# Performance work log

Hardware: AMD Instinct MI355X
Metric: run time of the kernel (lower is better)

Reference implementation:

```python
import jax, jax.numpy as jnp
import numpy as np

N_NODES = 50000
N_EDGES = 800000
N_GRAPHS = 2500
IN_DIM = 128
HID = 64
HEADS = 2
NEG_SLOPE = 0.2


def _gat_layer(x, W, att_src, att_dst, bias, src, dst, n):
    # W: [F_in, H*C], att_*: [H, C], bias: [C]
    h = (x @ W).reshape(n, HEADS, HID)            # [N,H,C]
    a_src = jnp.sum(h * att_src[None], axis=-1)   # [N,H]
    a_dst = jnp.sum(h * att_dst[None], axis=-1)   # [N,H]
    e = jax.nn.leaky_relu(a_src[src] + a_dst[dst], NEG_SLOPE)  # [E,H]
    # segment softmax over destination neighborhoods
    m = jax.ops.segment_max(e, dst, num_segments=n)            # [N,H]
    m = jnp.where(jnp.isfinite(m), m, 0.0)
    ex = jnp.exp(e - m[dst])
    s = jax.ops.segment_sum(ex, dst, num_segments=n)           # [N,H]
    alpha = ex / jnp.maximum(s[dst], 1e-16)                    # [E,H]
    msg = h[src] * alpha[:, :, None]                           # [E,H,C]
    out = jax.ops.segment_sum(msg, dst, num_segments=n)        # [N,H,C]
    return out.mean(axis=1) + bias                             # concat=False -> head mean


def _with_self_loops(edge_index, n):
    loop = jnp.arange(n, dtype=edge_index.dtype)
    src = jnp.concatenate([edge_index[0], loop])
    dst = jnp.concatenate([edge_index[1], loop])
    return src, dst


def setup_inputs() -> dict:
    key = jax.random.key(0)
    ks = jax.random.split(key, 16)
    x = jax.random.normal(ks[0], (N_NODES, IN_DIM), dtype=jnp.float32)
    edge_index = jax.random.randint(ks[1], (2, N_EDGES), 0, N_NODES, dtype=jnp.int32)
    batch = jnp.sort(jax.random.randint(ks[2], (N_NODES,), 0, N_GRAPHS, dtype=jnp.int32))

    def glorot(k, shape):
        fan = shape[0] + shape[-1]
        return jax.random.normal(k, shape, dtype=jnp.float32) * np.sqrt(2.0 / fan)

    inp = {"x": x, "edge_index": edge_index, "batch": batch}
    dims = [IN_DIM, HID, HID]
    for i in range(3):
        inp[f"W{i+1}"] = glorot(ks[3 + 4 * i], (dims[i], HEADS * HID))
        inp[f"att_src{i+1}"] = glorot(ks[4 + 4 * i], (HEADS, HID))
        inp[f"att_dst{i+1}"] = glorot(ks[5 + 4 * i], (HEADS, HID))
        inp[f"b{i+1}"] = jnp.zeros((HID,), dtype=jnp.float32)
    inp["lin_w"] = glorot(ks[15], (HID, 1))
    inp["lin_b"] = jnp.zeros((1,), dtype=jnp.float32)
    return inp


def reference(x, W1, att_src1, att_dst1, b1, W2, att_src2, att_dst2, b2,
              W3, att_src3, att_dst3, b3, lin_w, lin_b, edge_index, batch):
    n = x.shape[0]
    src, dst = _with_self_loops(edge_index, n)
    h = jax.nn.relu(_gat_layer(x, W1, att_src1, att_dst1, b1, src, dst, n))
    h = jax.nn.relu(_gat_layer(h, W2, att_src2, att_dst2, b2, src, dst, n))
    h = jax.nn.relu(_gat_layer(h, W3, att_src3, att_dst3, b3, src, dst, n))
    # global mean pool over graphs
    sums = jax.ops.segment_sum(h, batch, num_segments=N_GRAPHS)          # [G,C]
    cnt = jax.ops.segment_sum(jnp.ones((n,), h.dtype), batch, num_segments=N_GRAPHS)
    pooled = sums / jnp.maximum(cnt, 1.0)[:, None]
    return pooled @ lin_w + lin_b                                        # [G,1]
```

## Files before the change

kernel.cpp:

```cpp
#include <hip/hip_runtime.h>
#include <hip/hip_fp16.h>
#include <math.h>


__device__ __forceinline__ float lrelu(float v) { return v > 0.f ? v : 0.2f * v; }

__device__ __forceinline__ float wave_max(float v) {
  for (int off = 32; off; off >>= 1) v = fmaxf(v, __shfl_xor(v, off, 64));
  return v;
}
__device__ __forceinline__ float half_sum(float v) {
  for (int off = 16; off; off >>= 1) v += __shfl_xor(v, off, 64);
  return v;
}
__device__ __forceinline__ float half_max(float v) {
  for (int off = 16; off; off >>= 1) v = fmaxf(v, __shfl_xor(v, off, 64));
  return v;
}

__global__ void count_rank(const int* __restrict__ ei, int* __restrict__ deg,
                           int* __restrict__ rank, int e) {
  int j0 = blockIdx.x * 1024 + threadIdx.x;
#pragma unroll
  for (int k = 0; k < 4; ++k) {
    int j = j0 + k * 256;
    if (j < e) rank[j] = atomicAdd(&deg[ei[e + j]], 1);
  }
}

__global__ void scan_blocks(const int* __restrict__ deg, int* __restrict__ row_ptr,
                            int* __restrict__ btot, int n) {
  __shared__ int sm[256];
  int i = blockIdx.x * 256 + threadIdx.x;
  int v = (i < n) ? deg[i] : 0;
  sm[threadIdx.x] = v;
  __syncthreads();
  for (int off = 1; off < 256; off <<= 1) {
    int t = (threadIdx.x >= off) ? sm[threadIdx.x - off] : 0;
    __syncthreads();
    sm[threadIdx.x] += t;
    __syncthreads();
  }
  if (i < n) row_ptr[i] = sm[threadIdx.x] - v;
  if (threadIdx.x == 255) btot[blockIdx.x] = sm[255];
}

__global__ void scan_totals(int* __restrict__ btot, int nb) {
  __shared__ int sm[256];
  int v = (threadIdx.x < nb) ? btot[threadIdx.x] : 0;
  sm[threadIdx.x] = v;
  __syncthreads();
  for (int off = 1; off < 256; off <<= 1) {
    int t = (threadIdx.x >= off) ? sm[threadIdx.x - off] : 0;
    __syncthreads();
    sm[threadIdx.x] += t;
    __syncthreads();
  }
  if (threadIdx.x < nb) btot[threadIdx.x] = sm[threadIdx.x] - v;
}

__global__ void scan_add(int* __restrict__ row_ptr, int* __restrict__ csr,
                         const int* __restrict__ btot, int n, int total) {
  int i = blockIdx.x * 256 + threadIdx.x;
  if (i < n) {
    int v = row_ptr[i] + btot[blockIdx.x] + i;
    row_ptr[i] = v;
    csr[v] = i;
  }
  if (i == 0) row_ptr[n] = total;
}

__global__ void place_kernel(const int* __restrict__ ei, const int* __restrict__ rank,
                             const int* __restrict__ row_ptr, int* __restrict__ csr,
                             int e) {
  int j0 = blockIdx.x * 1024 + threadIdx.x;
#pragma unroll
  for (int k = 0; k < 4; ++k) {
    int j = j0 + k * 256;
    if (j < e) {
      int d = ei[e + j];
      csr[row_ptr[d] + 1 + rank[j]] = ei[j];
    }
  }
}

template <int K>
__global__ __launch_bounds__(256) void gemm_att(const float* __restrict__ X,
                                                const float* __restrict__ W,
                                                const float* __restrict__ asw,
                                                const float* __restrict__ adw,
                                                __half* __restrict__ H16,
                                                float* __restrict__ a_src,
                                                float* __restrict__ a_dst, int N) {
  __shared__ float Xs[64 * 68];
  int tid = threadIdx.x;
  int row0 = blockIdx.x * 64;
  int head = blockIdx.y;
  int cgrp = tid & 15;
  int rg = tid >> 4;
  int c0 = head * 64 + cgrp * 4;
  float acc[4][4] = {};

  for (int kc = 0; kc < K; kc += 64) {
    for (int idx = tid; idx < 64 * 64; idx += 256) {
      int r = idx >> 6;
      int k = idx & 63;
      int gr = row0 + r;
      if (gr >= N) gr = N - 1;
      Xs[r * 68 + k] = X[(size_t)gr * K + kc + k];
    }
    __syncthreads();

    const float* wp = W + (size_t)kc * 128 + c0;
#pragma unroll 2
    for (int k = 0; k < 64; k += 4) {
      float4 xr[4];
#pragma unroll
      for (int j = 0; j < 4; ++j)
        xr[j] = *(const float4*)(&Xs[(rg * 4 + j) * 68 + k]);
#pragma unroll
      for (int kk = 0; kk < 4; ++kk) {
        float4 w4 = *(const float4*)(wp + (k + kk) * 128);
#pragma unroll
        for (int j = 0; j < 4; ++j) {
          float xv = ((const float*)&xr[j])[kk];
          acc[j][0] = fmaf(xv, w4.x, acc[j][0]);
          acc[j][1] = fmaf(xv, w4.y, acc[j][1]);
          acc[j][2] = fmaf(xv, w4.z, acc[j][2]);
          acc[j][3] = fmaf(xv, w4.w, acc[j][3]);
        }
      }
    }
    __syncthreads();
  }

  float4 aw = *(const float4*)(asw + c0);
  float4 dw = *(const float4*)(adw + c0);
#pragma unroll
  for (int j = 0; j < 4; ++j) {
    int r = row0 + rg * 4 + j;
    float sp = acc[j][0] * aw.x + acc[j][1] * aw.y + acc[j][2] * aw.z + acc[j][3] * aw.w;
    float dp = acc[j][0] * dw.x + acc[j][1] * dw.y + acc[j][2] * dw.z + acc[j][3] * dw.w;
#pragma unroll
    for (int off = 1; off < 16; off <<= 1) {
      sp += __shfl_xor(sp, off, 64);
      dp += __shfl_xor(dp, off, 64);
    }
    if (r < N) {
      union { __half2 h2[2]; uint2 u; } pk;
      pk.h2[0] = __floats2half2_rn(acc[j][0], acc[j][1]);
      pk.h2[1] = __floats2half2_rn(acc[j][2], acc[j][3]);
      *(uint2*)(H16 + (size_t)r * 128 + c0) = pk.u;
      if (cgrp == 0) {
        a_src[r * 2 + head] = sp;
        a_dst[r * 2 + head] = dp;
      }
    }
  }
}

__device__ __forceinline__ void ld_grp8(const __half* __restrict__ H16, int half_,
                                        int c8, int headsel, int sub, int s,
                                        float p0, float p1, int g,
                                        uint4* h, float* q) {
#pragma unroll
  for (int k = 0; k < 4; ++k) {
    int idx = half_ + g * 8 + k * 2 + sub;
    int st = __shfl(s, idx, 64);
    float q0 = __shfl(p0, idx, 64);
    float q1 = __shfl(p1, idx, 64);
    q[k] = headsel ? q1 : q0;
    h[k] = *(const uint4*)(H16 + (size_t)st * 128 + c8);
  }
}
__device__ __forceinline__ void fma_grp8(const uint4* h, const float* q,
                                         float* acc) {
#pragma unroll
  for (int k = 0; k < 4; ++k) {
    union { uint u; __half2 h2; } a, b, c, d;
    a.u = h[k].x; b.u = h[k].y; c.u = h[k].z; d.u = h[k].w;
    float2 f0 = __half22float2(a.h2);
    float2 f1 = __half22float2(b.h2);
    float2 f2 = __half22float2(c.h2);
    float2 f3 = __half22float2(d.h2);
    acc[0] = fmaf(f0.x, q[k], acc[0]);
    acc[1] = fmaf(f0.y, q[k], acc[1]);
    acc[2] = fmaf(f1.x, q[k], acc[2]);
    acc[3] = fmaf(f1.y, q[k], acc[3]);
    acc[4] = fmaf(f2.x, q[k], acc[4]);
    acc[5] = fmaf(f2.y, q[k], acc[5]);
    acc[6] = fmaf(f3.x, q[k], acc[6]);
    acc[7] = fmaf(f3.y, q[k], acc[7]);
  }
}
__device__ __forceinline__ void gather_pipe8(const __half* __restrict__ H16, int half_,
                                             int c8, int headsel, int sub, int s,
                                             float p0, float p1, int maxcnt,
                                             float* acc) {
  int groups = (maxcnt + 7) >> 3;
  uint4 ha[4], hb[4];
  float qa[4], qb[4];
  ld_grp8(H16, half_, c8, headsel, sub, s, p0, p1, 0, ha, qa);
  int g = 1;
  for (; g + 1 < groups; g += 2) {
    ld_grp8(H16, half_, c8, headsel, sub, s, p0, p1, g, hb, qb);
    fma_grp8(ha, qa, acc);
    ld_grp8(H16, half_, c8, headsel, sub, s, p0, p1, g + 1, ha, qa);
    fma_grp8(hb, qb, acc);
  }
  if (g < groups) {
    ld_grp8(H16, half_, c8, headsel, sub, s, p0, p1, g, hb, qb);
    fma_grp8(ha, qa, acc);
    fma_grp8(hb, qb, acc);
  } else {
    fma_grp8(ha, qa, acc);
  }
}

template <int POOL>
__global__ __launch_bounds__(256) void aggregate_fused(
    const __half* __restrict__ H16, const float* __restrict__ a_src,
    const float* __restrict__ a_dst, const float* __restrict__ bias,
    const int* __restrict__ row_ptr, const int* __restrict__ csr,
    float* __restrict__ out, const float* __restrict__ lw,
    float* __restrict__ pvn, int N) {
  int lane = threadIdx.x & 63;
  int half_ = lane & 32;
  int l32 = lane & 31;
  int dst = blockIdx.x * 8 + ((threadIdx.x >> 6) << 1) + (half_ >> 5);
  bool live = dst < N;
  int beg = live ? row_ptr[dst] : 0;
  int end = live ? row_ptr[dst + 1] : 0;
  int cnt = end - beg;
  float2 ad = live ? ((const float2*)a_dst)[dst] : make_float2(0.f, 0.f);
  int sub = l32 >> 4;
  int m = l32 & 15;
  int c8 = m * 8;
  int headsel = m >> 3;
  float acc[8] = {};
  float inv0, inv1;

  int maxcnt = (int)wave_max((float)cnt);
  if (maxcnt < 1) maxcnt = 1;

  if (maxcnt <= 32) {
    int j = beg + l32;
    bool valid = l32 < cnt;
    int s = valid ? csr[j] : 0;
    float2 as = ((const float2*)a_src)[s];
    float e0 = valid ? lrelu(as.x + ad.x) : -1e30f;
    float e1 = valid ? lrelu(as.y + ad.y) : -1e30f;
    float m0 = half_max(e0);
    float m1 = half_max(e1);
    float p0 = __expf(e0 - m0);
    float p1 = __expf(e1 - m1);
    inv0 = 1.f / fmaxf(half_sum(valid ? p0 : 0.f), 1e-16f);
    inv1 = 1.f / fmaxf(half_sum(valid ? p1 : 0.f), 1e-16f);
    gather_pipe8(H16, half_, c8, headsel, sub, s, p0, p1, maxcnt, acc);
  } else {
    float m0 = -1e30f, m1 = -1e30f, s0 = 0.f, s1 = 0.f;
    for (int base = 0; base < maxcnt; base += 32) {
      int j = beg + base + l32;
      bool valid = (base + l32) < cnt;
      int s = valid ? csr[j] : 0;
      float2 as = ((const float2*)a_src)[s];
      float e0 = valid ? lrelu(as.x + ad.x) : -1e30f;
      float e1 = valid ? lrelu(as.y + ad.y) : -1e30f;
      float nm0 = fmaxf(m0, half_max(e0));
      float nm1 = fmaxf(m1, half_max(e1));
      s0 = s0 * __expf(m0 - nm0) + half_sum(valid ? __expf(e0 - nm0) : 0.f);
      s1 = s1 * __expf(m1 - nm1) + half_sum(valid ? __expf(e1 - nm1) : 0.f);
      m0 = nm0; m1 = nm1;
    }
    inv0 = 1.f / fmaxf(s0, 1e-16f);
    inv1 = 1.f / fmaxf(s1, 1e-16f);
    for (int base = 0; base < maxcnt; base += 32) {
      int j = beg + base + l32;
      bool valid = (base + l32) < cnt;
      int s = valid ? csr[j] : 0;
      float2 as = ((const float2*)a_src)[s];
      float e0 = valid ? lrelu(as.x + ad.x) : -1e30f;
      float e1 = valid ? lrelu(as.y + ad.y) : -1e30f;
      float p0 = __expf(e0 - m0);
      float p1 = __expf(e1 - m1);
      int rem = maxcnt - base;
      if (rem > 32) rem = 32;
      gather_pipe8(H16, half_, c8, headsel, sub, s, p0, p1, rem, acc);
    }
  }

#pragma unroll
  for (int j = 0; j < 8; ++j) acc[j] += __shfl_xor(acc[j], 16, 64);

  float il = headsel ? inv1 : inv0;
  float v[8], w[8];
#pragma unroll
  for (int j = 0; j < 8; ++j) v[j] = acc[j] * il;
#pragma unroll
  for (int j = 0; j < 8; ++j) w[j] = __shfl_xor(v[j], 8, 64);

  if (m < 8 && sub == 0 && live) {
    int c = m * 8;
    float4 b0 = *(const float4*)(bias + c);
    float4 b1 = *(const float4*)(bias + c + 4);
    float r[8];
    r[0] = fmaxf(0.5f * (v[0] + w[0]) + b0.x, 0.f);
    r[1] = fmaxf(0.5f * (v[1] + w[1]) + b0.y, 0.f);
    r[2] = fmaxf(0.5f * (v[2] + w[2]) + b0.z, 0.f);
    r[3] = fmaxf(0.5f * (v[3] + w[3]) + b0.w, 0.f);
    r[4] = fmaxf(0.5f * (v[4] + w[4]) + b1.x, 0.f);
    r[5] = fmaxf(0.5f * (v[5] + w[5]) + b1.y, 0.f);
    r[6] = fmaxf(0.5f * (v[6] + w[6]) + b1.z, 0.f);
    r[7] = fmaxf(0.5f * (v[7] + w[7]) + b1.w, 0.f);
    if (POOL) {
      float4 l0 = *(const float4*)(lw + c);
      float4 l1 = *(const float4*)(lw + c + 4);
      float pv = r[0] * l0.x + r[1] * l0.y + r[2] * l0.z + r[3] * l0.w +
                 r[4] * l1.x + r[5] * l1.y + r[6] * l1.z + r[7] * l1.w;
      pv += __shfl_xor(pv, 1, 64);
      pv += __shfl_xor(pv, 2, 64);
      pv += __shfl_xor(pv, 4, 64);
      if (m == 0) pvn[dst] = pv;
    } else {
      *(float4*)(out + (size_t)dst * 64 + c) = make_float4(r[0], r[1], r[2], r[3]);
      *(float4*)(out + (size_t)dst * 64 + c + 4) = make_float4(r[4], r[5], r[6], r[7]);
    }
  }
}

__device__ __forceinline__ int lower_bound(const int* __restrict__ a, int n, int key) {
  int lo = 0, hi = n;
  while (lo < hi) {
    int mid = (lo + hi) >> 1;
    if (a[mid] < key) lo = mid + 1; else hi = mid;
  }
  return lo;
}

__global__ void finalize_kernel(const float* __restrict__ pvn,
                                const int* __restrict__ batch,
                                const float* __restrict__ lb,
                                float* __restrict__ out, int N, int G) {
  int g = blockIdx.x * blockDim.x + threadIdx.x;
  if (g >= G) return;
  int lo = lower_bound(batch, N, g);
  int hi = lower_bound(batch, N, g + 1);
  float s = 0.f;
  for (int i = lo; i < hi; ++i) s += pvn[i];
  out[g] = s / fmaxf((float)(hi - lo), 1.f) + lb[0];
}

extern "C" void kernel_launch(void* const* d_in, const int* in_sizes, int n_in,
                              void* d_out, int out_size, void* d_ws, size_t ws_size,
                              hipStream_t stream) {
  const float* x   = (const float*)d_in[0];
  const int* ei    = (const int*)d_in[1];
  const int* batch = (const int*)d_in[2];
  const float* W1  = (const float*)d_in[3];
  const float* as1 = (const float*)d_in[4];
  const float* ad1 = (const float*)d_in[5];
  const float* b1  = (const float*)d_in[6];
  const float* W2  = (const float*)d_in[7];
  const float* as2 = (const float*)d_in[8];
  const float* ad2 = (const float*)d_in[9];
  const float* b2  = (const float*)d_in[10];
  const float* W3  = (const float*)d_in[11];
  const float* as3 = (const float*)d_in[12];
  const float* ad3 = (const float*)d_in[13];
  const float* b3  = (const float*)d_in[14];
  const float* lw  = (const float*)d_in[15];
  const float* lb  = (const float*)d_in[16];
  float* out = (float*)d_out;

  const int N = in_sizes[0] / 128;
  const int E = in_sizes[1] / 2;
  const int ET = N + E;
  const int G = out_size;
  const int NB = (N + 255) / 256;

  char* p = (char*)d_ws;
  auto take = [&](size_t bytes) {
    char* r = p;
    p += (bytes + 255) & ~(size_t)255;
    return r;
  };
  int* deg      = (int*)take((size_t)N * 4);
  int* row_ptr  = (int*)take((size_t)(N + 1) * 4);
  int* rank     = (int*)take((size_t)E * 4);
  int* btot     = (int*)take((size_t)NB * 4);
  int* csr      = (int*)take((size_t)ET * 4);
  __half* H16   = (__half*)take((size_t)N * 128 * 2);
  float* a_src  = (float*)take((size_t)N * 2 * 4);
  float* a_dst  = (float*)take((size_t)N * 2 * 4);
  float* bufA   = (float*)take((size_t)N * 64 * 4);
  float* bufB   = (float*)take((size_t)N * 64 * 4);
  float* pvn    = (float*)take((size_t)N * 4);
  (void)ws_size; (void)n_in;

  hipMemsetAsync(deg, 0, (size_t)N * 4, stream);
  count_rank<<<(E + 1023) / 1024, 256, 0, stream>>>(ei, deg, rank, E);
  scan_blocks<<<NB, 256, 0, stream>>>(deg, row_ptr, btot, N);
  scan_totals<<<1, 256, 0, stream>>>(btot, NB);
  scan_add<<<NB, 256, 0, stream>>>(row_ptr, csr, btot, N, ET);
  place_kernel<<<(E + 1023) / 1024, 256, 0, stream>>>(ei, rank, row_ptr, csr, E);

  const dim3 gblk((N + 63) / 64, 2);
  const int ablk = (N + 7) / 8;

  gemm_att<128><<<gblk, 256, 0, stream>>>(x, W1, as1, ad1, H16, a_src, a_dst, N);
  aggregate_fused<0><<<ablk, 256, 0, stream>>>(H16, a_src, a_dst, b1, row_ptr, csr,
                                               bufA, lw, pvn, N);
  gemm_att<64><<<gblk, 256, 0, stream>>>(bufA, W2, as2, ad2, H16, a_src, a_dst, N);
  aggregate_fused<0><<<ablk, 256, 0, stream>>>(H16, a_src, a_dst, b2, row_ptr, csr,
                                               bufB, lw, pvn, N);
  gemm_att<64><<<gblk, 256, 0, stream>>>(bufB, W3, as3, ad3, H16, a_src, a_dst, N);
  aggregate_fused<1><<<ablk, 256, 0, stream>>>(H16, a_src, a_dst, b3, row_ptr, csr,
                                               bufA, lw, pvn, N);

  finalize_kernel<<<(G + 255) / 256, 256, 0, stream>>>(pvn, batch, lb, out, N, G);
}
```

Baseline: 349.7 us.

## Fuse layer-1 GEMM with degree counting and shrink GEMM row tile to 32

The first-layer GEMM and the edge degree/rank counting now run in one launch: the first blocks compute the GEMM tiles and the remaining blocks do the atomic counting. This removes a kernel launch and lets the compute-bound GEMM overlap with the atomic-heavy counting. All GEMMs also move from 64-row to 32-row tiles, which halves per-thread accumulators and doubles block count for more parallelism. The cost is lower register-level reuse of W loads per row.

```diff
diff --git a/kernel.cpp b/kernel.cpp
--- a/kernel.cpp
+++ b/kernel.cpp
@@ -18,14 +18,105 @@
   return v;
 }
 
-__global__ void count_rank(const int* __restrict__ ei, int* __restrict__ deg,
-                           int* __restrict__ rank, int e) {
-  int j0 = blockIdx.x * 1024 + threadIdx.x;
-#pragma unroll
-  for (int k = 0; k < 4; ++k) {
-    int j = j0 + k * 256;
-    if (j < e) rank[j] = atomicAdd(&deg[ei[e + j]], 1);
-  }
+template <int K>
+__device__ __forceinline__ void gemm_body(
+    int bx, int head, const float* __restrict__ X, const float* __restrict__ W,
+    const float* __restrict__ asw, const float* __restrict__ adw,
+    __half* __restrict__ H16, float* __restrict__ a_src,
+    float* __restrict__ a_dst, int N, float* Xs) {
+  int tid = threadIdx.x;
+  int row0 = bx * 32;
+  int cgrp = tid & 15;
+  int rowid = tid >> 4;
+  int c0 = head * 64 + cgrp * 4;
+  float acc[2][4] = {};
+
+  for (int kc = 0; kc < K; kc += 64) {
+    for (int idx = tid; idx < 32 * 64; idx += 256) {
+      int r = idx >> 6;
+      int k = idx & 63;
+      int gr = row0 + r;
+      if (gr >= N) gr = N - 1;
+      Xs[r * 68 + k] = X[(size_t)gr * K + kc + k];
+    }
+    __syncthreads();
+
+    const float* wp = W + (size_t)kc * 128 + c0;
+#pragma unroll 2
+    for (int k = 0; k < 64; k += 4) {
+      float4 xr[2];
+#pragma unroll
+      for (int j = 0; j < 2; ++j)
+        xr[j] = *(const float4*)(&Xs[(rowid * 2 + j) * 68 + k]);
+#pragma unroll
+      for (int kk = 0; kk < 4; ++kk) {
+        float4 w4 = *(const float4*)(wp + (k + kk) * 128);
+#pragma unroll
+        for (int j = 0; j < 2; ++j) {
+          float xv = ((const float*)&xr[j])[kk];
+          acc[j][0] = fmaf(xv, w4.x, acc[j][0]);
+          acc[j][1] = fmaf(xv, w4.y, acc[j][1]);
+          acc[j][2] = fmaf(xv, w4.z, acc[j][2]);
+          acc[j][3] = fmaf(xv, w4.w, acc[j][3]);
+        }
+      }
+    }
+    __syncthreads();
+  }
+
+  float4 aw = *(const float4*)(asw + c0);
+  float4 dw = *(const float4*)(adw + c0);
+#pragma unroll
+  for (int j = 0; j < 2; ++j) {
+    int r = row0 + rowid * 2 + j;
+    float sp = acc[j][0] * aw.x + acc[j][1] * aw.y + acc[j][2] * aw.z + acc[j][3] * aw.w;
+    float dp = acc[j][0] * dw.x + acc[j][1] * dw.y + acc[j][2] * dw.z + acc[j][3] * dw.w;
+#pragma unroll
+    for (int off = 1; off < 16; off <<= 1) {
+      sp += __shfl_xor(sp, off, 64);
+      dp += __shfl_xor(dp, off, 64);
+    }
+    if (r < N) {
+      union { __half2 h2[2]; uint2 u; } pk;
+      pk.h2[0] = __floats2half2_rn(acc[j][0], acc[j][1]);
+      pk.h2[1] = __floats2half2_rn(acc[j][2], acc[j][3]);
+      *(uint2*)(H16 + (size_t)r * 128 + c0) = pk.u;
+      if (cgrp == 0) {
+        a_src[r * 2 + head] = sp;
+        a_dst[r * 2 + head] = dp;
+      }
+    }
+  }
+}
+
+__global__ __launch_bounds__(256) void k1_gemm_count(
+    const float* __restrict__ X, const float* __restrict__ W,
+    const float* __restrict__ asw, const float* __restrict__ adw,
+    __half* __restrict__ H16, float* __restrict__ a_src,
+    float* __restrict__ a_dst, const int* __restrict__ ei,
+    int* __restrict__ deg, int* __restrict__ rank, int N, int E, int GV) {
+  __shared__ float Xs[32 * 68];
+  int bid = blockIdx.x;
+  if (bid < GV) {
+    gemm_body<128>(bid >> 1, bid & 1, X, W, asw, adw, H16, a_src, a_dst, N, Xs);
+  } else {
+    int j0 = (bid - GV) * 1024 + threadIdx.x;
+#pragma unroll
+    for (int k = 0; k < 4; ++k) {
+      int j = j0 + k * 256;
+      if (j < E) rank[j] = atomicAdd(&deg[ei[E + j]], 1);
+    }
+  }
+}
+
+template <int K>
+__global__ __launch_bounds__(256) void gemm_kernel(
+    const float* __restrict__ X, const float* __restrict__ W,
+    const float* __restrict__ asw, const float* __restrict__ adw,
+    __half* __restrict__ H16, float* __restrict__ a_src,
+    float* __restrict__ a_dst, int N) {
+  __shared__ float Xs[32 * 68];
+  gemm_body<K>(blockIdx.x, blockIdx.y, X, W, asw, adw, H16, a_src, a_dst, N, Xs);
 }
 
 __global__ void scan_blocks(const int* __restrict__ deg, int* __restrict__ row_ptr,
@@ -80,81 +171,6 @@
     if (j < e) {
       int d = ei[e + j];
       csr[row_ptr[d] + 1 + rank[j]] = ei[j];
-    }
-  }
-}
-
-template <int K>
-__global__ __launch_bounds__(256) void gemm_att(const float* __restrict__ X,
-                                                const float* __restrict__ W,
-                                                const float* __restrict__ asw,
-                                                const float* __restrict__ adw,
-                                                __half* __restrict__ H16,
-                                                float* __restrict__ a_src,
-                                                float* __restrict__ a_dst, int N) {
-  __shared__ float Xs[64 * 68];
-  int tid = threadIdx.x;
-  int row0 = blockIdx.x * 64;
-  int head = blockIdx.y;
-  int cgrp = tid & 15;
-  int rg = tid >> 4;
-  int c0 = head * 64 + cgrp * 4;
-  float acc[4][4] = {};
-
-  for (int kc = 0; kc < K; kc += 64) {
-    for (int idx = tid; idx < 64 * 64; idx += 256) {
-      int r = idx >> 6;
-      int k = idx & 63;
-      int gr = row0 + r;
-      if (gr >= N) gr = N - 1;
-      Xs[r * 68 + k] = X[(size_t)gr * K + kc + k];
-    }
-    __syncthreads();
-
-    const float* wp = W + (size_t)kc * 128 + c0;
-#pragma unroll 2
-    for (int k = 0; k < 64; k += 4) {
-      float4 xr[4];
-#pragma unroll
-      for (int j = 0; j < 4; ++j)
-        xr[j] = *(const float4*)(&Xs[(rg * 4 + j) * 68 + k]);
-#pragma unroll
-      for (int kk = 0; kk < 4; ++kk) {
-        float4 w4 = *(const float4*)(wp + (k + kk) * 128);
-#pragma unroll
-        for (int j = 0; j < 4; ++j) {
-          float xv = ((const float*)&xr[j])[kk];
-          acc[j][0] = fmaf(xv, w4.x, acc[j][0]);
-          acc[j][1] = fmaf(xv, w4.y, acc[j][1]);
-          acc[j][2] = fmaf(xv, w4.z, acc[j][2]);
-          acc[j][3] = fmaf(xv, w4.w, acc[j][3]);
-        }
-      }
-    }
-    __syncthreads();
-  }
-
-  float4 aw = *(const float4*)(asw + c0);
-  float4 dw = *(const float4*)(adw + c0);
-#pragma unroll
-  for (int j = 0; j < 4; ++j) {
-    int r = row0 + rg * 4 + j;
-    float sp = acc[j][0] * aw.x + acc[j][1] * aw.y + acc[j][2] * aw.z + acc[j][3] * aw.w;
-    float dp = acc[j][0] * dw.x + acc[j][1] * dw.y + acc[j][2] * dw.z + acc[j][3] * dw.w;
-#pragma unroll
-    for (int off = 1; off < 16; off <<= 1) {
-      sp += __shfl_xor(sp, off, 64);
-      dp += __shfl_xor(dp, off, 64);
-    }
-    if (r < N) {
-      union { __half2 h2[2]; uint2 u; } pk;
-      pk.h2[0] = __floats2half2_rn(acc[j][0], acc[j][1]);
-      pk.h2[1] = __floats2half2_rn(acc[j][2], acc[j][3]);
-      *(uint2*)(H16 + (size_t)r * 128 + c0) = pk.u;
-      if (cgrp == 0) {
-        a_src[r * 2 + head] = sp;
-        a_dst[r * 2 + head] = dp;
-      }
     }
   }
 }
@@ -397,23 +413,26 @@
   float* pvn    = (float*)take((size_t)N * 4);
   (void)ws_size; (void)n_in;
 
+  const int nb32 = (N + 31) / 32;
+  const int GV = nb32 * 2;
+  const int CV = (E + 1023) / 1024;
+  const dim3 gblk2(nb32, 2);
+  const int ablk = (N + 7) / 8;
+
   hipMemsetAsync(deg, 0, (size_t)N * 4, stream);
-  count_rank<<<(E + 1023) / 1024, 256, 0, stream>>>(ei, deg, rank, E);
+  k1_gemm_count<<<GV + CV, 256, 0, stream>>>(x, W1, as1, ad1, H16, a_src,
+                                             a_dst, ei, deg, rank, N, E, GV);
   scan_blocks<<<NB, 256, 0, stream>>>(deg, row_ptr, btot, N);
   scan_totals<<<1, 256, 0, stream>>>(btot, NB);
   scan_add<<<NB, 256, 0, stream>>>(row_ptr, csr, btot, N, ET);
   place_kernel<<<(E + 1023) / 1024, 256, 0, stream>>>(ei, rank, row_ptr, csr, E);
 
-  const dim3 gblk((N + 63) / 64, 2);
-  const int ablk = (N + 7) / 8;
-
-  gemm_att<128><<<gblk, 256, 0, stream>>>(x, W1, as1, ad1, H16, a_src, a_dst, N);
   aggregate_fused<0><<<ablk, 256, 0, stream>>>(H16, a_src, a_dst, b1, row_ptr, csr,
                                                bufA, lw, pvn, N);
-  gemm_att<64><<<gblk, 256, 0, stream>>>(bufA, W2, as2, ad2, H16, a_src, a_dst, N);
+  gemm_kernel<64><<<gblk2, 256, 0, stream>>>(bufA, W2, as2, ad2, H16, a_src, a_dst, N);
   aggregate_fused<0><<<ablk, 256, 0, stream>>>(H16, a_src, a_dst, b2, row_ptr, csr,
                                                bufB, lw, pvn, N);
-  gemm_att<64><<<gblk, 256, 0, stream>>>(bufB, W3, as3, ad3, H16, a_src, a_dst, N);
+  gemm_kernel<64><<<gblk2, 256, 0, stream>>>(bufB, W3, as3, ad3, H16, a_src, a_dst, N);
   aggregate_fused<1><<<ablk, 256, 0, stream>>>(H16, a_src, a_dst, b3, row_ptr, csr,
                                                bufA, lw, pvn, N);
 
```

After: 371.1 us. 1.06x slower.
